# Kernel optimization log

Hardware: AMD Instinct MI355X
Metric: run time of the kernel (lower is better)

Reference implementation:

```python
import jax, jax.numpy as jnp
import numpy as np

B, S, D, E, K, NS = 4, 1024, 1024, 8, 2, 2
H = 4 * D
TEMP = 0.1
SCALE = 0.02


def setup_inputs() -> dict:
    key = jax.random.key(0)
    ks = jax.random.split(key, 12)
    f32 = jnp.float32
    return {
        "x": jax.random.normal(ks[0], (B, S, D), f32),
        "Ws1": jax.random.normal(ks[1], (NS, D, H), f32) * SCALE,
        "bs1": jnp.zeros((NS, H), f32),
        "Ws2": jax.random.normal(ks[2], (NS, H, D), f32) * SCALE,
        "bs2": jnp.zeros((NS, D), f32),
        "We1": jax.random.normal(ks[3], (E, D, H), f32) * SCALE,
        "be1": jnp.zeros((E, H), f32),
        "We2": jax.random.normal(ks[4], (E, H, D), f32) * SCALE,
        "be2": jnp.zeros((E, D), f32),
        "Wr": jax.random.normal(ks[5], (D, E), f32) * SCALE,
        "br": jnp.zeros((E,), f32),
        "gumbel": jax.random.gumbel(ks[6], (B, S, E), f32),
    }


def reference(x, Ws1, bs1, Ws2, bs2, We1, be1, We2, be2, Wr, br, gumbel):
    act = jax.nn.gelu
    # shared experts: dense FFN per shared expert, summed over experts
    hs = act(jnp.einsum('bsd,edh->ebsh', x, Ws1) + bs1[:, None, None, :])
    shared_sum = (jnp.einsum('ebsh,ehd->ebsd', hs, Ws2)
                  + bs2[:, None, None, :]).sum(axis=0)  # [B,S,D]
    # routing experts: ALL experts computed densely over all tokens
    he = act(jnp.einsum('bsd,edh->ebsh', x, We1) + be1[:, None, None, :])
    all_experts = jnp.einsum('ebsh,ehd->ebsd', he, We2) + be2[:, None, None, :]  # [E,B,S,D]
    # router + gumbel-softmax top-k selection
    logits = x @ Wr + br                                  # [B,S,E]
    router_probs = jax.nn.softmax((logits + gumbel) / TEMP, axis=-1)
    chosen = jax.lax.top_k(router_probs, K)[1]            # [B,S,K] int
    one_hot = jax.nn.one_hot(chosen, E, dtype=x.dtype)    # [B,S,K,E]
    # unweighted sum of selected experts' outputs (sum over k and experts)
    out = jnp.einsum('bske,ebsd->bsd', one_hot, all_experts)
    return out + shared_sum
```

## Files before the change

### kernel.cpp

```cpp
#include <hip/hip_runtime.h>
#include <cstdint>
#include <cstddef>

#define T_TOK 4096
#define DDIM 1024
#define HDIM 4096
#define NEXP 8
#define NSHARED 2

typedef unsigned short ushort_t;
typedef __attribute__((ext_vector_type(8))) short short8;
typedef __attribute__((ext_vector_type(4))) float f32x4;

__device__ inline ushort_t f2bf(float f) {
  unsigned u = __float_as_uint(f);
  u += 0x7fffu + ((u >> 16) & 1u);
  return (ushort_t)(u >> 16);
}

__device__ inline void async_copy16(const ushort_t* g, ushort_t* l) {
  __builtin_amdgcn_global_load_lds(
      (const __attribute__((address_space(1))) void*)g,
      (__attribute__((address_space(3))) void*)l, 16, 0, 0);
}

__device__ inline float gelu_tanh(float x) {
  float u = 0.7978845608028654f * (x + 0.044715f * x * x * x);
  float th = 1.0f - 2.0f / (__expf(2.0f * u) + 1.0f);
  return 0.5f * x * (1.0f + th);
}

__global__ __launch_bounds__(256) void router_kernel(
    const float* __restrict__ x, const float* __restrict__ Wr,
    const float* __restrict__ br, const float* __restrict__ gum,
    int* __restrict__ choice, int* __restrict__ cnt) {
  int lane = threadIdx.x & 63;
  int wv = blockIdx.x * 4 + (threadIdx.x >> 6);
  if (wv >= T_TOK) return;
  const float* xr = x + (long)wv * DDIM;
  float acc[NEXP] = {0.f, 0.f, 0.f, 0.f, 0.f, 0.f, 0.f, 0.f};
  for (int d = lane; d < DDIM; d += 64) {
    float xv = xr[d];
    const float* w = Wr + d * NEXP;
#pragma unroll
    for (int e = 0; e < NEXP; e++) acc[e] += xv * w[e];
  }
#pragma unroll
  for (int e = 0; e < NEXP; e++) {
    float v = acc[e];
#pragma unroll
    for (int o = 32; o > 0; o >>= 1) v += __shfl_down(v, o);
    acc[e] = v;
  }
  if (lane == 0) {
    float vals[NEXP];
#pragma unroll
    for (int e = 0; e < NEXP; e++) vals[e] = acc[e] + br[e] + gum[(long)wv * NEXP + e];
    int i1 = 0; float b1 = vals[0];
#pragma unroll
    for (int e = 1; e < NEXP; e++) if (vals[e] > b1) { b1 = vals[e]; i1 = e; }
    int i2 = -1; float b2 = -3.4e38f;
#pragma unroll
    for (int e = 0; e < NEXP; e++) if (e != i1 && vals[e] > b2) { b2 = vals[e]; i2 = e; }
    choice[wv] = i1 | (i2 << 4);
    atomicAdd(&cnt[i1], 1);
    atomicAdd(&cnt[i2], 1);
  }
}

__global__ void prefix_kernel(const int* __restrict__ cnt, int* __restrict__ base,
                              int* __restrict__ fill) {
  if (threadIdx.x == 0 && blockIdx.x == 0) {
    int off = 0;
    for (int e = 0; e < NEXP; e++) {
      base[e] = off;
      off += (cnt[e] + 127) & ~127;
      fill[e] = 0;
    }
  }
}

__global__ __launch_bounds__(256) void scatter_kernel(
    const int* __restrict__ choice, const int* __restrict__ base,
    int* __restrict__ fill, int* __restrict__ idx) {
  int t = blockIdx.x * 256 + threadIdx.x;
  if (t >= T_TOK) return;
  int c = choice[t];
  int e1 = c & 15, e2 = (c >> 4) & 15;
  int p1 = atomicAdd(&fill[e1], 1);
  idx[base[e1] + p1] = t;
  int p2 = atomicAdd(&fill[e2], 1);
  idx[base[e2] + p2] = t;
}

__global__ __launch_bounds__(256) void cast_x_kernel(
    const float* __restrict__ in, ushort_t* __restrict__ out, int n4) {
  int i = blockIdx.x * 256 + threadIdx.x;
  if (i >= n4) return;
  float4 v = ((const float4*)in)[i];
  ushort4 o = make_ushort4(f2bf(v.x), f2bf(v.y), f2bf(v.z), f2bf(v.w));
  ((ushort4*)out)[i] = o;
}

__global__ __launch_bounds__(256) void transpose_cast(
    const float* __restrict__ in, ushort_t* __restrict__ out, int R, int C) {
  __shared__ float tile[32][33];
  long zoff = (long)blockIdx.z * R * C;
  in += zoff; out += zoff;
  int c0 = blockIdx.x * 32, r0 = blockIdx.y * 32;
  int tx = threadIdx.x, ty = threadIdx.y;
#pragma unroll
  for (int k = 0; k < 4; k++)
    tile[ty + 8 * k][tx] = in[(long)(r0 + ty + 8 * k) * C + (c0 + tx)];
  __syncthreads();
#pragma unroll
  for (int k = 0; k < 4; k++)
    out[(long)(c0 + ty + 8 * k) * R + (r0 + tx)] = f2bf(tile[tx][ty + 8 * k]);
}

__global__ __launch_bounds__(256) void gemm1_kernel(
    const ushort_t* __restrict__ xb, const ushort_t* __restrict__ W1t,
    const float* __restrict__ bs1, const float* __restrict__ be1,
    ushort_t* __restrict__ h_sh, ushort_t* __restrict__ h_rt,
    const int* __restrict__ cnt, const int* __restrict__ base,
    const int* __restrict__ idx) {
  __shared__ ushort_t As[2 * 128 * 32];
  __shared__ ushort_t Bs[2 * 128 * 32];

  int tid = threadIdx.x;
  int z = blockIdx.z;
  int row0 = blockIdx.y * 128, col0 = blockIdx.x * 128;
  bool sh = (z < NSHARED);

  int e = 0, M = T_TOK, base_e = 0;
  const ushort_t* Bp;
  const float* bias;
  if (sh) {
    Bp = W1t + (size_t)z * HDIM * DDIM;
    bias = bs1 + (size_t)z * HDIM;
  } else {
    e = z - NSHARED; M = cnt[e];
    if (row0 >= M) return;
    base_e = base[e];
    Bp = W1t + (size_t)(NSHARED + e) * HDIM * DDIM;
    bias = be1 + (size_t)e * HDIM;
  }

  int tq = tid & 3, tr = tid >> 2;
  const ushort_t *aS, *aS2;
  if (sh) {
    aS = xb + (size_t)(row0 + tr) * DDIM + tq * 8;
    aS2 = aS + (size_t)64 * DDIM;
  } else {
    int s1 = row0 + tr;      if (s1 > M - 1) s1 = M - 1;
    int s2 = row0 + tr + 64; if (s2 > M - 1) s2 = M - 1;
    aS  = xb + (size_t)idx[base_e + s1] * DDIM + tq * 8;
    aS2 = xb + (size_t)idx[base_e + s2] * DDIM + tq * 8;
  }
  const ushort_t* bS = Bp + (size_t)(col0 + tr) * DDIM + tq * 8;
  const ushort_t* bS2 = bS + (size_t)64 * DDIM;
  ushort_t* aD = As + tid * 8;
  ushort_t* bD = Bs + tid * 8;

  int lane = tid & 63, wv = tid >> 6;
  int wr = wv >> 1, wc = wv & 1;
  int ln = lane & 15, quad = lane >> 4;
  f32x4 acc[4][4] = {};
  const ushort_t* aLds = As + (wr * 64 + ln) * 32 + quad * 8;
  const ushort_t* bLds = Bs + (wc * 64 + ln) * 32 + quad * 8;

  for (int k0 = 0; k0 < DDIM; k0 += 64) {
    async_copy16(aS, aD);            async_copy16(aS2, aD + 2048);
    async_copy16(aS + 32, aD + 4096); async_copy16(aS2 + 32, aD + 6144);
    async_copy16(bS, bD);            async_copy16(bS2, bD + 2048);
    async_copy16(bS + 32, bD + 4096); async_copy16(bS2 + 32, bD + 6144);
    __syncthreads();
#pragma unroll
    for (int s = 0; s < 2; s++) {
      short8 af[4], bf[4];
#pragma unroll
      for (int i = 0; i < 4; i++) {
        af[i] = *(const short8*)(aLds + s * 4096 + i * 16 * 32);
        bf[i] = *(const short8*)(bLds + s * 4096 + i * 16 * 32);
      }
#pragma unroll
      for (int i = 0; i < 4; i++)
#pragma unroll
        for (int j = 0; j < 4; j++)
          acc[i][j] = __builtin_amdgcn_mfma_f32_16x16x32_bf16(af[i], bf[j],
                                                              acc[i][j], 0, 0, 0);
    }
    __syncthreads();
    aS += 64; aS2 += 64; bS += 64; bS2 += 64;
  }

#pragma unroll
  for (int i = 0; i < 4; i++) {
    int rowB = row0 + wr * 64 + i * 16 + quad * 4;
#pragma unroll
    for (int j = 0; j < 4; j++) {
      int col = col0 + wc * 64 + j * 16 + ln;
      float b = bias[col];
#pragma unroll
      for (int r = 0; r < 4; r++) {
        int t = rowB + r;
        float v = gelu_tanh(acc[i][j][r] + b);
        if (sh) {
          h_sh[(size_t)t * (2 * HDIM) + (size_t)z * HDIM + col] = f2bf(v);
        } else if (t < M) {
          h_rt[((size_t)base_e + t) * HDIM + col] = f2bf(v);
        }
      }
    }
  }
}

__global__ __launch_bounds__(256) void gemm2_kernel(
    const ushort_t* __restrict__ h_sh, const ushort_t* __restrict__ h_rt,
    const ushort_t* __restrict__ W2t, const float* __restrict__ bs2,
    const float* __restrict__ be2, float* __restrict__ outF,
    const int* __restrict__ cnt, const int* __restrict__ base,
    const int* __restrict__ idx) {
  __shared__ ushort_t As[2 * 128 * 32];
  __shared__ ushort_t Bs[2 * 128 * 32];

  int tid = threadIdx.x;
  int z = blockIdx.z;
  int row0 = blockIdx.y * 128, col0 = blockIdx.x * 128;
  bool sh = (z < NSHARED);

  int e = 0, M = T_TOK, base_e = 0;
  const ushort_t* Ap;
  const ushort_t* Bp;
  long lda;
  if (sh) {
    Ap = h_sh + (size_t)z * HDIM;
    lda = 2 * HDIM;
    Bp = W2t + (size_t)z * DDIM * HDIM;
  } else {
    e = z - NSHARED; M = cnt[e];
    if (row0 >= M) return;
    base_e = base[e];
    Ap = h_rt + (size_t)base_e * HDIM;
    lda = HDIM;
    Bp = W2t + (size_t)(NSHARED + e) * DDIM * HDIM;
  }

  int tq = tid & 3, tr = tid >> 2;
  const ushort_t* aS = Ap + (long)(row0 + tr) * lda + tq * 8;
  const ushort_t* aS2 = aS + 64L * lda;
  const ushort_t* bS = Bp + (size_t)(col0 + tr) * HDIM + tq * 8;
  const ushort_t* bS2 = bS + (size_t)64 * HDIM;
  ushort_t* aD = As + tid * 8;
  ushort_t* bD = Bs + tid * 8;

  int lane = tid & 63, wv = tid >> 6;
  int wr = wv >> 1, wc = wv & 1;
  int ln = lane & 15, quad = lane >> 4;
  f32x4 acc[4][4] = {};
  const ushort_t* aLds = As + (wr * 64 + ln) * 32 + quad * 8;
  const ushort_t* bLds = Bs + (wc * 64 + ln) * 32 + quad * 8;

  for (int k0 = 0; k0 < HDIM; k0 += 64) {
    async_copy16(aS, aD);            async_copy16(aS2, aD + 2048);
    async_copy16(aS + 32, aD + 4096); async_copy16(aS2 + 32, aD + 6144);
    async_copy16(bS, bD);            async_copy16(bS2, bD + 2048);
    async_copy16(bS + 32, bD + 4096); async_copy16(bS2 + 32, bD + 6144);
    __syncthreads();
#pragma unroll
    for (int s = 0; s < 2; s++) {
      short8 af[4], bf[4];
#pragma unroll
      for (int i = 0; i < 4; i++) {
        af[i] = *(const short8*)(aLds + s * 4096 + i * 16 * 32);
        bf[i] = *(const short8*)(bLds + s * 4096 + i * 16 * 32);
      }
#pragma unroll
      for (int i = 0; i < 4; i++)
#pragma unroll
        for (int j = 0; j < 4; j++)
          acc[i][j] = __builtin_amdgcn_mfma_f32_16x16x32_bf16(af[i], bf[j],
                                                              acc[i][j], 0, 0, 0);
    }
    __syncthreads();
    aS += 64; aS2 += 64; bS += 64; bS2 += 64;
  }

#pragma unroll
  for (int i = 0; i < 4; i++) {
    int rowB = row0 + wr * 64 + i * 16 + quad * 4;
#pragma unroll
    for (int j = 0; j < 4; j++) {
      int col = col0 + wc * 64 + j * 16 + ln;
      float b;
      if (sh)
        b = (z == 0) ? (bs2[col] + bs2[DDIM + col]) : 0.0f;
      else
        b = be2[(size_t)e * DDIM + col];
#pragma unroll
      for (int r = 0; r < 4; r++) {
        int t = rowB + r;
        float v = acc[i][j][r] + b;
        if (sh) {
          atomicAdd(outF + (size_t)t * DDIM + col, v);
        } else if (t < M) {
          int tok = idx[base_e + t];
          atomicAdd(outF + (size_t)tok * DDIM + col, v);
        }
      }
    }
  }
}

extern "C" void kernel_launch(void* const* d_in, const int* in_sizes, int n_in,
                              void* d_out, int out_size, void* d_ws,
                              size_t ws_size, hipStream_t stream) {
  const float* x   = (const float*)d_in[0];
  const float* Ws1 = (const float*)d_in[1];
  const float* bs1 = (const float*)d_in[2];
  const float* Ws2 = (const float*)d_in[3];
  const float* bs2 = (const float*)d_in[4];
  const float* We1 = (const float*)d_in[5];
  const float* be1 = (const float*)d_in[6];
  const float* We2 = (const float*)d_in[7];
  const float* be2 = (const float*)d_in[8];
  const float* Wr  = (const float*)d_in[9];
  const float* br  = (const float*)d_in[10];
  const float* gum = (const float*)d_in[11];
  float* out = (float*)d_out;

  char* ws = (char*)d_ws;
  size_t off = 0;
  int* cnt    = (int*)(ws + off); off += 256;
  int* base   = (int*)(ws + off); off += 256;
  int* fill   = (int*)(ws + off); off += 256;
  int* choice = (int*)(ws + off); off += T_TOK * 4;
  int* idx    = (int*)(ws + off); off += 9216 * 4;
  off = (off + 255) & ~(size_t)255;
  ushort_t* xb   = (ushort_t*)(ws + off); off += (size_t)T_TOK * DDIM * 2;
  ushort_t* W1t  = (ushort_t*)(ws + off); off += (size_t)10 * HDIM * DDIM * 2;
  ushort_t* W2t  = (ushort_t*)(ws + off); off += (size_t)10 * DDIM * HDIM * 2;
  ushort_t* h_sh = (ushort_t*)(ws + off); off += (size_t)T_TOK * 2 * HDIM * 2;
  ushort_t* h_rt = (ushort_t*)(ws + off); off += (size_t)9216 * HDIM * 2;
  (void)ws_size;

  hipMemsetAsync(out, 0, (size_t)T_TOK * DDIM * sizeof(float), stream);
  hipMemsetAsync(cnt, 0, 256, stream);

  router_kernel<<<T_TOK / 4, 256, 0, stream>>>(x, Wr, br, gum, choice, cnt);
  prefix_kernel<<<1, 64, 0, stream>>>(cnt, base, fill);
  scatter_kernel<<<T_TOK / 256, 256, 0, stream>>>(choice, base, fill, idx);
  cast_x_kernel<<<(T_TOK * DDIM / 4 + 255) / 256, 256, 0, stream>>>(
      x, xb, T_TOK * DDIM / 4);

  transpose_cast<<<dim3(HDIM / 32, DDIM / 32, NSHARED), dim3(32, 8), 0, stream>>>(
      Ws1, W1t, DDIM, HDIM);
  transpose_cast<<<dim3(HDIM / 32, DDIM / 32, NEXP), dim3(32, 8), 0, stream>>>(
      We1, W1t + (size_t)NSHARED * HDIM * DDIM, DDIM, HDIM);
  transpose_cast<<<dim3(DDIM / 32, HDIM / 32, NSHARED), dim3(32, 8), 0, stream>>>(
      Ws2, W2t, HDIM, DDIM);
  transpose_cast<<<dim3(DDIM / 32, HDIM / 32, NEXP), dim3(32, 8), 0, stream>>>(
      We2, W2t + (size_t)NSHARED * DDIM * HDIM, HDIM, DDIM);

  gemm1_kernel<<<dim3(HDIM / 128, T_TOK / 128, NSHARED + NEXP), 256, 0, stream>>>(
      xb, W1t, bs1, be1, h_sh, h_rt, cnt, base, idx);
  gemm2_kernel<<<dim3(DDIM / 128, T_TOK / 128, NSHARED + NEXP), 256, 0, stream>>>(
      h_sh, h_rt, W2t, bs2, be2, out, cnt, base, idx);

  (void)in_sizes; (void)n_in; (void)out_size;
}
```

Measured before the change: 1.162 ms.

## Replace gemm2 atomics with per-expert stores and a combine kernel; swizzle tiles

```diff
diff --git a/kernel.cpp b/kernel.cpp
--- a/kernel.cpp
+++ b/kernel.cpp
@@ -7,6 +7,7 @@
 #define HDIM 4096
 #define NEXP 8
 #define NSHARED 2
+#define RT_CAP 9216
 
 typedef unsigned short ushort_t;
 typedef __attribute__((ext_vector_type(8))) short short8;
@@ -28,6 +29,13 @@
   float u = 0.7978845608028654f * (x + 0.044715f * x * x * x);
   float th = 1.0f - 2.0f / (__expf(2.0f * u) + 1.0f);
   return 0.5f * x * (1.0f + th);
+}
+
+__device__ inline void swizzle_xy(int* bx, int* by) {
+  int l = blockIdx.x + gridDim.x * blockIdx.y;
+  int g = l >> 8;
+  *bx = (l & 7) + (g << 3);
+  *by = (l >> 3) & 31;
 }
 
 __global__ __launch_bounds__(256) void router_kernel(
@@ -82,15 +90,15 @@
 
 __global__ __launch_bounds__(256) void scatter_kernel(
     const int* __restrict__ choice, const int* __restrict__ base,
-    int* __restrict__ fill, int* __restrict__ idx) {
+    int* __restrict__ fill, int* __restrict__ idx, int* __restrict__ pos) {
   int t = blockIdx.x * 256 + threadIdx.x;
   if (t >= T_TOK) return;
   int c = choice[t];
   int e1 = c & 15, e2 = (c >> 4) & 15;
-  int p1 = atomicAdd(&fill[e1], 1);
-  idx[base[e1] + p1] = t;
-  int p2 = atomicAdd(&fill[e2], 1);
-  idx[base[e2] + p2] = t;
+  int p1 = base[e1] + atomicAdd(&fill[e1], 1);
+  idx[p1] = t; pos[2 * t] = p1;
+  int p2 = base[e2] + atomicAdd(&fill[e2], 1);
+  idx[p2] = t; pos[2 * t + 1] = p2;
 }
 
 __global__ __launch_bounds__(256) void cast_x_kernel(
@@ -102,11 +110,14 @@
   ((ushort4*)out)[i] = o;
 }
 
-__global__ __launch_bounds__(256) void transpose_cast(
-    const float* __restrict__ in, ushort_t* __restrict__ out, int R, int C) {
+__global__ __launch_bounds__(256) void transpose_cast10(
+    const float* __restrict__ inS, const float* __restrict__ inE,
+    ushort_t* __restrict__ out, int R, int C) {
   __shared__ float tile[32][33];
-  long zoff = (long)blockIdx.z * R * C;
-  in += zoff; out += zoff;
+  int z = blockIdx.z;
+  const float* in = (z < NSHARED) ? inS + (size_t)z * R * C
+                                  : inE + (size_t)(z - NSHARED) * R * C;
+  ushort_t* op = out + (size_t)z * R * C;
   int c0 = blockIdx.x * 32, r0 = blockIdx.y * 32;
   int tx = threadIdx.x, ty = threadIdx.y;
 #pragma unroll
@@ -115,7 +126,7 @@
   __syncthreads();
 #pragma unroll
   for (int k = 0; k < 4; k++)
-    out[(long)(c0 + ty + 8 * k) * R + (r0 + tx)] = f2bf(tile[tx][ty + 8 * k]);
+    op[(long)(c0 + ty + 8 * k) * R + (r0 + tx)] = f2bf(tile[tx][ty + 8 * k]);
 }
 
 __global__ __launch_bounds__(256) void gemm1_kernel(
@@ -129,7 +140,8 @@
 
   int tid = threadIdx.x;
   int z = blockIdx.z;
-  int row0 = blockIdx.y * 128, col0 = blockIdx.x * 128;
+  int bx, by; swizzle_xy(&bx, &by);
+  int row0 = by * 128, col0 = bx * 128;
   bool sh = (z < NSHARED);
 
   int e = 0, M = T_TOK, base_e = 0;
@@ -170,9 +182,9 @@
   const ushort_t* bLds = Bs + (wc * 64 + ln) * 32 + quad * 8;
 
   for (int k0 = 0; k0 < DDIM; k0 += 64) {
-    async_copy16(aS, aD);            async_copy16(aS2, aD + 2048);
+    async_copy16(aS, aD);             async_copy16(aS2, aD + 2048);
     async_copy16(aS + 32, aD + 4096); async_copy16(aS2 + 32, aD + 6144);
-    async_copy16(bS, bD);            async_copy16(bS2, bD + 2048);
+    async_copy16(bS, bD);             async_copy16(bS2, bD + 2048);
     async_copy16(bS + 32, bD + 4096); async_copy16(bS2 + 32, bD + 6144);
     __syncthreads();
 #pragma unroll
@@ -217,26 +229,28 @@
 
 __global__ __launch_bounds__(256) void gemm2_kernel(
     const ushort_t* __restrict__ h_sh, const ushort_t* __restrict__ h_rt,
-    const ushort_t* __restrict__ W2t, const float* __restrict__ bs2,
-    const float* __restrict__ be2, float* __restrict__ outF,
-    const int* __restrict__ cnt, const int* __restrict__ base,
-    const int* __restrict__ idx) {
+    const ushort_t* __restrict__ W2t, float* __restrict__ outShA,
+    float* __restrict__ outShB, float* __restrict__ outRt,
+    const int* __restrict__ cnt, const int* __restrict__ base) {
   __shared__ ushort_t As[2 * 128 * 32];
   __shared__ ushort_t Bs[2 * 128 * 32];
 
   int tid = threadIdx.x;
   int z = blockIdx.z;
-  int row0 = blockIdx.y * 128, col0 = blockIdx.x * 128;
+  int bx, by; swizzle_xy(&bx, &by);
+  int row0 = by * 128, col0 = bx * 128;
   bool sh = (z < NSHARED);
 
   int e = 0, M = T_TOK, base_e = 0;
   const ushort_t* Ap;
+  long lda;
   const ushort_t* Bp;
-  long lda;
+  float* outP;
   if (sh) {
     Ap = h_sh + (size_t)z * HDIM;
     lda = 2 * HDIM;
     Bp = W2t + (size_t)z * DDIM * HDIM;
+    outP = (z == 0) ? outShA : outShB;
   } else {
     e = z - NSHARED; M = cnt[e];
     if (row0 >= M) return;
@@ -244,6 +258,7 @@
     Ap = h_rt + (size_t)base_e * HDIM;
     lda = HDIM;
     Bp = W2t + (size_t)(NSHARED + e) * DDIM * HDIM;
+    outP = outRt + (size_t)base_e * DDIM;
   }
 
   int tq = tid & 3, tr = tid >> 2;
@@ -262,9 +277,9 @@
   const ushort_t* bLds = Bs + (wc * 64 + ln) * 32 + quad * 8;
 
   for (int k0 = 0; k0 < HDIM; k0 += 64) {
-    async_copy16(aS, aD);            async_copy16(aS2, aD + 2048);
+    async_copy16(aS, aD);             async_copy16(aS2, aD + 2048);
     async_copy16(aS + 32, aD + 4096); async_copy16(aS2 + 32, aD + 6144);
-    async_copy16(bS, bD);            async_copy16(bS2, bD + 2048);
+    async_copy16(bS, bD);             async_copy16(bS2, bD + 2048);
     async_copy16(bS + 32, bD + 4096); async_copy16(bS2 + 32, bD + 6144);
     __syncthreads();
 #pragma unroll
@@ -292,24 +307,41 @@
 #pragma unroll
     for (int j = 0; j < 4; j++) {
       int col = col0 + wc * 64 + j * 16 + ln;
-      float b;
-      if (sh)
-        b = (z == 0) ? (bs2[col] + bs2[DDIM + col]) : 0.0f;
-      else
-        b = be2[(size_t)e * DDIM + col];
 #pragma unroll
       for (int r = 0; r < 4; r++) {
         int t = rowB + r;
-        float v = acc[i][j][r] + b;
-        if (sh) {
-          atomicAdd(outF + (size_t)t * DDIM + col, v);
-        } else if (t < M) {
-          int tok = idx[base_e + t];
-          atomicAdd(outF + (size_t)tok * DDIM + col, v);
-        }
+        if (sh || t < M) outP[(size_t)t * DDIM + col] = acc[i][j][r];
       }
     }
   }
+}
+
+__global__ __launch_bounds__(256) void combine_kernel(
+    const float* __restrict__ shA, const float* __restrict__ shB,
+    const float* __restrict__ rt, const float* __restrict__ bs2,
+    const float* __restrict__ be2, const int* __restrict__ choice,
+    const int* __restrict__ pos, float* __restrict__ out) {
+  int i = blockIdx.x * 256 + threadIdx.x;
+  int t = i >> 8;
+  int d4 = i & 255;
+  int c = choice[t];
+  int e1 = c & 15, e2 = (c >> 4) & 15;
+  long p1 = (long)pos[2 * t] * 256 + d4;
+  long p2 = (long)pos[2 * t + 1] * 256 + d4;
+  float4 a = ((const float4*)shA)[i];
+  float4 b = ((const float4*)shB)[i];
+  float4 r1 = ((const float4*)rt)[p1];
+  float4 r2 = ((const float4*)rt)[p2];
+  float4 b0 = ((const float4*)bs2)[d4];
+  float4 b1 = ((const float4*)bs2)[256 + d4];
+  float4 c1 = ((const float4*)be2)[e1 * 256 + d4];
+  float4 c2 = ((const float4*)be2)[e2 * 256 + d4];
+  float4 o;
+  o.x = a.x + b.x + r1.x + r2.x + b0.x + b1.x + c1.x + c2.x;
+  o.y = a.y + b.y + r1.y + r2.y + b0.y + b1.y + c1.y + c2.y;
+  o.z = a.z + b.z + r1.z + r2.z + b0.z + b1.z + c1.z + c2.z;
+  o.w = a.w + b.w + r1.w + r2.w + b0.w + b1.w + c1.w + c2.w;
+  ((float4*)out)[i] = o;
 }
 
 extern "C" void kernel_launch(void* const* d_in, const int* in_sizes, int n_in,
@@ -335,37 +367,37 @@
   int* base   = (int*)(ws + off); off += 256;
   int* fill   = (int*)(ws + off); off += 256;
   int* choice = (int*)(ws + off); off += T_TOK * 4;
-  int* idx    = (int*)(ws + off); off += 9216 * 4;
+  int* idx    = (int*)(ws + off); off += RT_CAP * 4;
+  int* pos    = (int*)(ws + off); off += T_TOK * 8;
   off = (off + 255) & ~(size_t)255;
   ushort_t* xb   = (ushort_t*)(ws + off); off += (size_t)T_TOK * DDIM * 2;
   ushort_t* W1t  = (ushort_t*)(ws + off); off += (size_t)10 * HDIM * DDIM * 2;
   ushort_t* W2t  = (ushort_t*)(ws + off); off += (size_t)10 * DDIM * HDIM * 2;
   ushort_t* h_sh = (ushort_t*)(ws + off); off += (size_t)T_TOK * 2 * HDIM * 2;
-  ushort_t* h_rt = (ushort_t*)(ws + off); off += (size_t)9216 * HDIM * 2;
+  ushort_t* h_rt = (ushort_t*)(ws + off); off += (size_t)RT_CAP * HDIM * 2;
+  float* outShA = (float*)W1t;
+  float* outShB = outShA + (size_t)T_TOK * DDIM;
+  float* outRt  = outShB + (size_t)T_TOK * DDIM;
   (void)ws_size;
 
-  hipMemsetAsync(out, 0, (size_t)T_TOK * DDIM * sizeof(float), stream);
   hipMemsetAsync(cnt, 0, 256, stream);
-
   router_kernel<<<T_TOK / 4, 256, 0, stream>>>(x, Wr, br, gum, choice, cnt);
   prefix_kernel<<<1, 64, 0, stream>>>(cnt, base, fill);
-  scatter_kernel<<<T_TOK / 256, 256, 0, stream>>>(choice, base, fill, idx);
+  scatter_kernel<<<T_TOK / 256, 256, 0, stream>>>(choice, base, fill, idx, pos);
   cast_x_kernel<<<(T_TOK * DDIM / 4 + 255) / 256, 256, 0, stream>>>(
       x, xb, T_TOK * DDIM / 4);
 
-  transpose_cast<<<dim3(HDIM / 32, DDIM / 32, NSHARED), dim3(32, 8), 0, stream>>>(
-      Ws1, W1t, DDIM, HDIM);
-  transpose_cast<<<dim3(HDIM / 32, DDIM / 32, NEXP), dim3(32, 8), 0, stream>>>(
-      We1, W1t + (size_t)NSHARED * HDIM * DDIM, DDIM, HDIM);
-  transpose_cast<<<dim3(DDIM / 32, HDIM / 32, NSHARED), dim3(32, 8), 0, stream>>>(
-      Ws2, W2t, HDIM, DDIM);
-  transpose_cast<<<dim3(DDIM / 32, HDIM / 32, NEXP), dim3(32, 8), 0, stream>>>(
-      We2, W2t + (size_t)NSHARED * DDIM * HDIM, HDIM, DDIM);
+  transpose_cast10<<<dim3(HDIM / 32, DDIM / 32, 10), dim3(32, 8), 0, stream>>>(
+      Ws1, We1, W1t, DDIM, HDIM);
+  transpose_cast10<<<dim3(DDIM / 32, HDIM / 32, 10), dim3(32, 8), 0, stream>>>(
+      Ws2, We2, W2t, HDIM, DDIM);
 
   gemm1_kernel<<<dim3(HDIM / 128, T_TOK / 128, NSHARED + NEXP), 256, 0, stream>>>(
       xb, W1t, bs1, be1, h_sh, h_rt, cnt, base, idx);
   gemm2_kernel<<<dim3(DDIM / 128, T_TOK / 128, NSHARED + NEXP), 256, 0, stream>>>(
-      h_sh, h_rt, W2t, bs2, be2, out, cnt, base, idx);
+      h_sh, h_rt, W2t, outShA, outShB, outRt, cnt, base);
+  combine_kernel<<<T_TOK * DDIM / 4 / 256, 256, 0, stream>>>(
+      outShA, outShB, outRt, bs2, be2, choice, pos, out);
 
   (void)in_sizes; (void)n_in; (void)out_size;
 }
```

After: 1.040 ms. 10.5% less time.
